# Performance work log

Hardware: AMD Instinct MI355X
Metric: run time of the kernel (lower is better)

Reference implementation:

```python
import jax, jax.numpy as jnp
import numpy as np

NEIGHBOR_RATE = 0.1  # neighbor_rate init arg
LEAKY_SLOPE = 0.2
NEG_INF = -1.0e9


def setup_inputs() -> dict:
    key = jax.random.key(0)
    k1, k2, k3, k4 = jax.random.split(key, 4)
    B, N, Din, H, hd = 4, 2048, 128, 4, 32  # output_dim = H*hd = 128
    h = jax.random.normal(k1, (B, N, Din), jnp.float32)
    adj = jax.random.uniform(k2, (B, N, N), jnp.float32)
    # stacked per-head params: W[k] in [Din, hd], a[k] in [2*hd]
    w_bound = 1.0 / np.sqrt(Din)
    a_bound = 1.0 / np.sqrt(2 * hd)
    W = jax.random.uniform(k3, (H, Din, hd), jnp.float32, -w_bound, w_bound)
    a = jax.random.uniform(k4, (H, 2 * hd), jnp.float32, -a_bound, a_bound)
    return {"h": h, "adj": adj, "W": W, "a": a}


def reference(h, adj, W, a):
    B, N, _ = h.shape
    H, _, hd = W.shape
    k = int(NEIGHBOR_RATE * N)  # num_neighbors
    # Wh: [B,H,N,hd]
    Wh = jnp.einsum('bnf,hfd->bhnd', h, W)
    # cat([Wh_i, Wh_j]) @ a  ==  Wh_i @ a[:hd] + Wh_j @ a[hd:] (broadcast trick)
    s_i = jnp.einsum('bhnd,hd->bhn', Wh, a[:, :hd])
    s_j = jnp.einsum('bhnd,hd->bhn', Wh, a[:, hd:])
    e = jax.nn.leaky_relu(s_i[..., :, None] + s_j[..., None, :], LEAKY_SLOPE)  # [B,H,N,N]
    # top-k mask along last (neighbor) axis, built by scatter like torch .scatter_
    _, idx = jax.lax.top_k(e, k)  # [B,H,N,k]
    row_mask = lambda i: jnp.zeros((N,), jnp.bool_).at[i].set(True)
    mask = jax.vmap(row_mask)(idx.reshape(-1, k)).reshape(e.shape)
    masked = jnp.where(mask, e, NEG_INF)
    attn = jax.nn.softmax(masked, axis=-1) * adj[:, None]  # [B,H,N,N]
    hp = jnp.einsum('bhnm,bhmd->bhnd', attn, Wh)
    # concat heads on feature dim -> [B,N,H*hd]
    return hp.transpose(0, 2, 1, 3).reshape(B, N, H * hd)
```

## Files before the change

### kernel.cpp

```cpp
#include <hip/hip_runtime.h>
#include <hip/hip_bf16.h>
#include <cmath>

#define BB 4
#define NN 2048
#define DIN 128
#define HH 4
#define HD 32
#define KSEL 204
#define BH (BB*HH)
#define KPAD 256
#define KST 264

typedef __attribute__((ext_vector_type(8))) short short8;
typedef __attribute__((ext_vector_type(4))) short short4v;
typedef __attribute__((ext_vector_type(4))) float float4v;

static __device__ inline short f2bf(float x) {
    __hip_bfloat16 b = __float2bfloat16(x);
    return __builtin_bit_cast(short, b);
}

typedef __attribute__((address_space(1))) const unsigned gq_t;
typedef __attribute__((address_space(3))) unsigned lq_t;
static __device__ inline void gload_lds16(const void* g, void* l) {
    __builtin_amdgcn_global_load_lds((gq_t*)g, (lq_t*)l, 16, 0, 0);
}

__global__ __launch_bounds__(256) void s_kernel(const float* __restrict__ h,
                                                const float* __restrict__ W,
                                                const float* __restrict__ a,
                                                float* __restrict__ si, float* __restrict__ sj) {
    __shared__ float w1L[HH][DIN], w2L[HH][DIN];
    int t = threadIdx.x;
    for (int e = t; e < 8 * DIN; e += 256) {
        int f = e & 127, v = e >> 7;
        int hh = v >> 1, half = v & 1;
        const float* Wp = W + ((size_t)hh * DIN + f) * HD;
        const float* ap = a + hh * 64 + half * 32;
        float acc = 0.f;
#pragma unroll
        for (int d = 0; d < 32; ++d) acc += Wp[d] * ap[d];
        if (half == 0) w1L[hh][f] = acc; else w2L[hh][f] = acc;
    }
    __syncthreads();

    int gid = blockIdx.x * 256 + t;
    int row = gid >> 2;
    int q   = gid & 3;
    int b = row >> 11, n = row & 2047;
    const float* hr = h + (size_t)row * DIN;

    float s1h0 = 0.f, s1h1 = 0.f, s1h2 = 0.f, s1h3 = 0.f;
    float s2h0 = 0.f, s2h1 = 0.f, s2h2 = 0.f, s2h3 = 0.f;
#pragma unroll
    for (int i = 0; i < 8; ++i) {
        int f = q * 4 + i * 16;
        float4 x = *(const float4*)(hr + f);
        const float* wa0 = &w1L[0][f]; const float* wb0 = &w2L[0][f];
        const float* wa1 = &w1L[1][f]; const float* wb1 = &w2L[1][f];
        const float* wa2 = &w1L[2][f]; const float* wb2 = &w2L[2][f];
        const float* wa3 = &w1L[3][f]; const float* wb3 = &w2L[3][f];
        s1h0 += x.x*wa0[0] + x.y*wa0[1] + x.z*wa0[2] + x.w*wa0[3];
        s2h0 += x.x*wb0[0] + x.y*wb0[1] + x.z*wb0[2] + x.w*wb0[3];
        s1h1 += x.x*wa1[0] + x.y*wa1[1] + x.z*wa1[2] + x.w*wa1[3];
        s2h1 += x.x*wb1[0] + x.y*wb1[1] + x.z*wb1[2] + x.w*wb1[3];
        s1h2 += x.x*wa2[0] + x.y*wa2[1] + x.z*wa2[2] + x.w*wa2[3];
        s2h2 += x.x*wb2[0] + x.y*wb2[1] + x.z*wb2[2] + x.w*wb2[3];
        s1h3 += x.x*wa3[0] + x.y*wa3[1] + x.z*wa3[2] + x.w*wa3[3];
        s2h3 += x.x*wb3[0] + x.y*wb3[1] + x.z*wb3[2] + x.w*wb3[3];
    }
#pragma unroll
    for (int off = 1; off <= 2; off <<= 1) {
        s1h0 += __shfl_xor(s1h0, off); s2h0 += __shfl_xor(s2h0, off);
        s1h1 += __shfl_xor(s1h1, off); s2h1 += __shfl_xor(s2h1, off);
        s1h2 += __shfl_xor(s1h2, off); s2h2 += __shfl_xor(s2h2, off);
        s1h3 += __shfl_xor(s1h3, off); s2h3 += __shfl_xor(s2h3, off);
    }
    float o1 = (q == 0) ? s1h0 : (q == 1) ? s1h1 : (q == 2) ? s1h2 : s1h3;
    float o2 = (q == 0) ? s2h0 : (q == 1) ? s2h1 : (q == 2) ? s2h2 : s2h3;
    size_t o = (size_t)(b * HH + q) * NN + n;
    si[o] = o1; sj[o] = o2;
}

__global__ __launch_bounds__(1024) void select_kernel(
        const float* __restrict__ h, const float* __restrict__ W,
        const float* __restrict__ sj,
        int* __restrict__ idxsel, float* __restrict__ sjsel,
        float* __restrict__ sjmax, short* __restrict__ Whsel) {
    int bh = blockIdx.x;
    int b = bh >> 2, hh = bh & 3;
    int t = threadIdx.x, lane = t & 63, w = t >> 6;
    __shared__ float sv[NN];
    __shared__ short WT[32][136];
    __shared__ int hist16[16][256];
    __shared__ int binInfo[2];
    __shared__ int wtot[4];
    __shared__ int wtotg[16], wtote[16], woffg[16], woffe[16];
    __shared__ float wmax[16];
    __shared__ int idxLDS[KSEL];

    for (int e = t; e < 32 * 128; e += 1024) {
        int n = e & 31, k = e >> 5;
        WT[n][k] = f2bf(W[(size_t)hh * (DIN * HD) + k * HD + n]);
    }

    const float* s = sj + (size_t)bh * NN;
    int j0 = t * 2;
    float2 xx = *(const float2*)(s + j0);
    sv[j0] = xx.x; sv[j0 + 1] = xx.y;
    unsigned u0 = __builtin_bit_cast(unsigned, xx.x);
    unsigned u1 = __builtin_bit_cast(unsigned, xx.y);
    u0 = (u0 & 0x80000000u) ? ~u0 : (u0 | 0x80000000u);
    u1 = (u1 & 0x80000000u) ? ~u1 : (u1 | 0x80000000u);
    float lmax = fmaxf(xx.x, xx.y);
#pragma unroll
    for (int off = 32; off >= 1; off >>= 1) lmax = fmaxf(lmax, __shfl_xor(lmax, off));
    if (lane == 0) wmax[w] = lmax;
    __syncthreads();
    if (t == 0) {
        float m = wmax[0];
#pragma unroll
        for (int i = 1; i < 16; ++i) m = fmaxf(m, wmax[i]);
        sjmax[bh] = m;
    }

    unsigned prefix = 0;
    int need = KSEL;
#pragma unroll
    for (int shift = 24; shift >= 0; shift -= 8) {
        ((int*)hist16)[t] = 0; ((int*)hist16)[t + 1024] = 0;
        ((int*)hist16)[t + 2048] = 0; ((int*)hist16)[t + 3072] = 0;
        __syncthreads();
        unsigned hmask = (shift < 24) ? (0xFFFFFFFFu << (shift + 8)) : 0u;
        if (((u0 ^ prefix) & hmask) == 0) atomicAdd(&hist16[w][(u0 >> shift) & 255], 1);
        if (((u1 ^ prefix) & hmask) == 0) atomicAdd(&hist16[w][(u1 >> shift) & 255], 1);
        __syncthreads();
        int sc = 0, hv = 0, bb = 0;
        if (t < 256) {
            bb = 255 - t;
            hv = 0;
#pragma unroll
            for (int i = 0; i < 16; ++i) hv += hist16[i][bb];
            sc = hv;
#pragma unroll
            for (int off = 1; off < 64; off <<= 1) {
                int u = __shfl_up(sc, off);
                if (lane >= off) sc += u;
            }
            if (lane == 63) wtot[w] = sc;
        }
        __syncthreads();
        if (t < 256) {
            int woffset = 0;
#pragma unroll
            for (int i = 0; i < 4; ++i) woffset += (i < w) ? wtot[i] : 0;
            int incl = sc + woffset;
            int excl = incl - hv;
            if (incl >= need && excl < need) {
                binInfo[0] = bb;
                binInfo[1] = excl;
            }
        }
        __syncthreads();
        prefix |= ((unsigned)binInfo[0]) << shift;
        need -= binInfo[1];
        __syncthreads();
    }
    unsigned T = prefix;
    int n_gt = KSEL - need;

    int cg = (u0 > T ? 1 : 0) + (u1 > T ? 1 : 0);
    int ce = (u0 == T ? 1 : 0) + (u1 == T ? 1 : 0);
    int sg = cg, se = ce;
#pragma unroll
    for (int off = 1; off < 64; off <<= 1) {
        int ug = __shfl_up(sg, off), ue = __shfl_up(se, off);
        if (lane >= off) { sg += ug; se += ue; }
    }
    if (lane == 63) { wtotg[w] = sg; wtote[w] = se; }
    __syncthreads();
    if (t == 0) {
        int rg = 0, re = 0;
#pragma unroll
        for (int i = 0; i < 16; ++i) {
            woffg[i] = rg; rg += wtotg[i];
            woffe[i] = re; re += wtote[i];
        }
    }
    __syncthreads();
    int pg = woffg[w] + sg - cg;
    int te = woffe[w] + se - ce;
    {
        unsigned kk[2] = {u0, u1};
#pragma unroll
        for (int r = 0; r < 2; ++r) {
            int j = j0 + r;
            if (kk[r] > T) {
                idxsel[bh * KSEL + pg] = j;
                sjsel[bh * KSEL + pg] = sv[j];
                idxLDS[pg] = j;
                pg++;
            } else if (kk[r] == T) {
                if (te < need) {
                    int pos = n_gt + te;
                    idxsel[bh * KSEL + pos] = j;
                    sjsel[bh * KSEL + pos] = sv[j];
                    idxLDS[pos] = j;
                }
                te++;
            }
        }
    }
    __syncthreads();

    {
        int mr = lane & 15, quad = lane >> 4;
        int jjp = w * 16 + mr;
        bool valid = jjp < KSEL;
        const float* hrow = h + ((size_t)b * NN + (valid ? idxLDS[jjp] : 0)) * DIN + quad * 8;
        float4v acc0 = {0.f, 0.f, 0.f, 0.f};
        float4v acc1 = {0.f, 0.f, 0.f, 0.f};
#pragma unroll
        for (int ks = 0; ks < 4; ++ks) {
            short8 afr;
            if (valid) {
                float4 xa = *(const float4*)(hrow + ks * 32);
                float4 xb = *(const float4*)(hrow + ks * 32 + 4);
                afr[0] = f2bf(xa.x); afr[1] = f2bf(xa.y); afr[2] = f2bf(xa.z); afr[3] = f2bf(xa.w);
                afr[4] = f2bf(xb.x); afr[5] = f2bf(xb.y); afr[6] = f2bf(xb.z); afr[7] = f2bf(xb.w);
            } else {
                afr = (short8){0, 0, 0, 0, 0, 0, 0, 0};
            }
            short8 b0 = *(const short8*)&WT[mr][ks * 32 + quad * 8];
            short8 b1 = *(const short8*)&WT[16 + mr][ks * 32 + quad * 8];
            acc0 = __builtin_amdgcn_mfma_f32_16x16x32_bf16(afr, b0, acc0, 0, 0, 0);
            acc1 = __builtin_amdgcn_mfma_f32_16x16x32_bf16(afr, b1, acc1, 0, 0, 0);
        }
        short4v o0, o1;
#pragma unroll
        for (int r = 0; r < 4; ++r) { o0[r] = f2bf(acc0[r]); o1[r] = f2bf(acc1[r]); }
        size_t base = (size_t)bh * HD * KPAD;
        int jjs = w * 16 + quad * 4;
        *(short4v*)&Whsel[base + (size_t)mr * KPAD + jjs] = o0;
        *(short4v*)&Whsel[base + (size_t)(16 + mr) * KPAD + jjs] = o1;
    }
}

__global__ __launch_bounds__(512) void attn2_kernel(
        const float* __restrict__ adj, const float* __restrict__ si,
        const int* __restrict__ idxsel, const float* __restrict__ sjsel,
        const float* __restrict__ sjmax, const short* __restrict__ Whsel,
        float* __restrict__ out) {
    int b = blockIdx.x >> 7;
    int tile = blockIdx.x & 127;
    __shared__ float adjbuf[2][2][NN];
    __shared__ short PSb[HH][16][KST];
    __shared__ int   idxS[HH][KPAD];
    __shared__ float sjS[HH][KPAD];
    __shared__ float invZS[HH][16];
    __shared__ float smaxS[HH];
    int t = threadIdx.x, w8 = t >> 6, lane = t & 63;
    int hh = w8 >> 1, g = w8 & 1;
    int mr = lane & 15, quad = lane >> 4;

    int i0 = tile * 16;
    const char* adjb = (const char*)(adj + (size_t)b * NN * NN + (size_t)i0 * NN);

    for (int e = t; e < HH * KPAD; e += 512) {
        int h2 = e >> 8, jj = e & 255;
        bool v = jj < KSEL;
        idxS[h2][jj] = v ? idxsel[(b * HH + h2) * KSEL + jj] : 0;
        sjS[h2][jj]  = v ? sjsel[(b * HH + h2) * KSEL + jj] : -1e30f;
    }
    if (t < HH) smaxS[t] = sjmax[b * HH + t];

    short8 bfr[8];
    {
        const short* wp = Whsel + (size_t)((b * HH + hh) * HD) * KPAD;
#pragma unroll
        for (int ks = 0; ks < 8; ++ks)
            bfr[ks] = *(const short8*)(wp + (size_t)(g * 16 + mr) * KPAD + ks * 32 + quad * 8);
    }
    int bh = b * HH + hh;
    float sivAll = (lane < 8) ? si[(size_t)bh * NN + i0 + 2 * lane + g] : 0.f;

    __syncthreads();

    {
        int lx = lane << 4, off = w8 << 10;
        gload_lds16(adjb + off + lx,              (char*)&adjbuf[0][0][0] + off);
        gload_lds16(adjb + 8192 + off + lx,       (char*)&adjbuf[0][0][0] + 8192 + off);
        gload_lds16(adjb + 16384 + off + lx,      (char*)&adjbuf[1][0][0] + off);
        gload_lds16(adjb + 24576 + off + lx,      (char*)&adjbuf[1][0][0] + 8192 + off);
    }
    asm volatile("s_waitcnt vmcnt(2)" ::: "memory");
    __builtin_amdgcn_sched_barrier(0);
    __builtin_amdgcn_s_barrier();

    float smax = smaxS[hh];
    for (int s = 0; s < 8; ++s) {
        int cur = s & 1;
        if (s >= 1 && s < 7) {
            const char* gs = adjb + (size_t)(s + 1) * 16384;
            char* lb = (char*)&adjbuf[cur ^ 1][0][0];
            int lx = lane << 4, off = w8 << 10;
            gload_lds16(gs + off + lx,        lb + off);
            gload_lds16(gs + 8192 + off + lx, lb + 8192 + off);
        }
        {
            int i_loc = 2 * s + g;
            float siv = __shfl(sivAll, s);
            float m = siv + smax;
            m = (m >= 0.f) ? m : 0.2f * m;
            float z = 0.f;
            short* prow = &PSb[hh][i_loc][0];
#pragma unroll
            for (int k = 0; k < 2; ++k) {
                int jj = k * 128 + lane * 2;
                int ja = idxS[hh][jj], jb = idxS[hh][jj + 1];
                float ava = adjbuf[cur][g][ja], avb = adjbuf[cur][g][jb];
                float ea = siv + sjS[hh][jj];
                float eb = siv + sjS[hh][jj + 1];
                ea = (ea >= 0.f) ? ea : 0.2f * ea;
                eb = (eb >= 0.f) ? eb : 0.2f * eb;
                float ca = __expf(ea - m);
                float cb = __expf(eb - m);
                z += ca + cb;
                short2 p;
                p.x = f2bf(ca * ava);
                p.y = f2bf(cb * avb);
                *(short2*)&prow[jj] = p;
            }
#pragma unroll
            for (int off = 32; off >= 1; off >>= 1) z += __shfl_xor(z, off);
            if (lane == 0) invZS[hh][i_loc] = 1.0f / z;
        }
        if (s < 7) {
            asm volatile("s_waitcnt vmcnt(0)" ::: "memory");
            __builtin_amdgcn_sched_barrier(0);
            __builtin_amdgcn_s_barrier();
        }
    }
    __syncthreads();

    {
        float4v acc = {0.f, 0.f, 0.f, 0.f};
#pragma unroll
        for (int ks = 0; ks < 8; ++ks) {
            short8 afr = *(const short8*)&PSb[hh][mr][ks * 32 + quad * 8];
            acc = __builtin_amdgcn_mfma_f32_16x16x32_bf16(afr, bfr[ks], acc, 0, 0, 0);
        }
#pragma unroll
        for (int r = 0; r < 4; ++r) {
            int i_loc = quad * 4 + r;
            int d = g * 16 + mr;
            out[((size_t)(b * NN + i0 + i_loc)) * (HH * HD) + hh * HD + d] =
                acc[r] * invZS[hh][i_loc];
        }
    }
}

extern "C" void kernel_launch(void* const* d_in, const int* in_sizes, int n_in,
                              void* d_out, int out_size, void* d_ws, size_t ws_size,
                              hipStream_t stream) {
    const float* h   = (const float*)d_in[0];
    const float* adj = (const float*)d_in[1];
    const float* W   = (const float*)d_in[2];
    const float* a   = (const float*)d_in[3];
    float* out = (float*)d_out;

    float* si     = (float*)d_ws;
    float* sj     = si + (size_t)BH * NN;
    float* sjsel  = sj + (size_t)BH * NN;
    float* sjmax  = sjsel + (size_t)BH * KSEL;
    int*   idxsel = (int*)(sjmax + 16);
    short* Whsel  = (short*)(idxsel + (size_t)BH * KSEL);

    s_kernel<<<128, 256, 0, stream>>>(h, W, a, si, sj);
    select_kernel<<<BH, 1024, 0, stream>>>(h, W, sj, idxsel, sjsel, sjmax, Whsel);
    attn2_kernel<<<BB * 128, 512, 0, stream>>>(adj, si, idxsel, sjsel, sjmax, Whsel, out);
}
```

Measured before the change: 126.5 us.

## Deepen adj prefetch to 4-slot ring, split rows across wave pair

Replaces the double-buffered two-row adj staging with a four-slot ring of single rows, keeping three loads in flight and waiting with graded vmcnt counts. Each row is now processed by both waves of a head, each handling half the selected neighbors, and the partial softmax denominators are combined at output time. The intent is to hide global-load latency better and spread the gather work more evenly. In exchange it runs twice as many barrier-separated steps and fully unrolls the loop.

```diff
diff --git a/kernel.cpp b/kernel.cpp
--- a/kernel.cpp
+++ b/kernel.cpp
@@ -254,11 +254,11 @@
         float* __restrict__ out) {
     int b = blockIdx.x >> 7;
     int tile = blockIdx.x & 127;
-    __shared__ float adjbuf[2][2][NN];
+    __shared__ float adjbuf[4][NN];
     __shared__ short PSb[HH][16][KST];
     __shared__ int   idxS[HH][KPAD];
     __shared__ float sjS[HH][KPAD];
-    __shared__ float invZS[HH][16];
+    __shared__ float zpartS[HH][16][2];
     __shared__ float smaxS[HH];
     int t = threadIdx.x, w8 = t >> 6, lane = t & 63;
     int hh = w8 >> 1, g = w8 & 1;
@@ -283,61 +283,55 @@
             bfr[ks] = *(const short8*)(wp + (size_t)(g * 16 + mr) * KPAD + ks * 32 + quad * 8);
     }
     int bh = b * HH + hh;
-    float sivAll = (lane < 8) ? si[(size_t)bh * NN + i0 + 2 * lane + g] : 0.f;
+    float sivAll = (lane < 16) ? si[(size_t)bh * NN + i0 + lane] : 0.f;
 
     __syncthreads();
 
     {
         int lx = lane << 4, off = w8 << 10;
-        gload_lds16(adjb + off + lx,              (char*)&adjbuf[0][0][0] + off);
-        gload_lds16(adjb + 8192 + off + lx,       (char*)&adjbuf[0][0][0] + 8192 + off);
-        gload_lds16(adjb + 16384 + off + lx,      (char*)&adjbuf[1][0][0] + off);
-        gload_lds16(adjb + 24576 + off + lx,      (char*)&adjbuf[1][0][0] + 8192 + off);
+        gload_lds16(adjb + off + lx,         (char*)&adjbuf[0][0] + off);
+        gload_lds16(adjb + 8192 + off + lx,  (char*)&adjbuf[1][0] + off);
+        gload_lds16(adjb + 16384 + off + lx, (char*)&adjbuf[2][0] + off);
     }
     asm volatile("s_waitcnt vmcnt(2)" ::: "memory");
     __builtin_amdgcn_sched_barrier(0);
     __builtin_amdgcn_s_barrier();
 
     float smax = smaxS[hh];
-    for (int s = 0; s < 8; ++s) {
-        int cur = s & 1;
-        if (s >= 1 && s < 7) {
-            const char* gs = adjb + (size_t)(s + 1) * 16384;
-            char* lb = (char*)&adjbuf[cur ^ 1][0][0];
+#pragma unroll
+    for (int s = 0; s < 16; ++s) {
+        int cur = s & 3;
+        if (s < 13) {
             int lx = lane << 4, off = w8 << 10;
-            gload_lds16(gs + off + lx,        lb + off);
-            gload_lds16(gs + 8192 + off + lx, lb + 8192 + off);
+            gload_lds16(adjb + (size_t)(s + 3) * 8192 + off + lx,
+                        (char*)&adjbuf[(s + 3) & 3][0] + off);
         }
         {
-            int i_loc = 2 * s + g;
             float siv = __shfl(sivAll, s);
             float m = siv + smax;
             m = (m >= 0.f) ? m : 0.2f * m;
-            float z = 0.f;
-            short* prow = &PSb[hh][i_loc][0];
-#pragma unroll
-            for (int k = 0; k < 2; ++k) {
-                int jj = k * 128 + lane * 2;
-                int ja = idxS[hh][jj], jb = idxS[hh][jj + 1];
-                float ava = adjbuf[cur][g][ja], avb = adjbuf[cur][g][jb];
-                float ea = siv + sjS[hh][jj];
-                float eb = siv + sjS[hh][jj + 1];
-                ea = (ea >= 0.f) ? ea : 0.2f * ea;
-                eb = (eb >= 0.f) ? eb : 0.2f * eb;
-                float ca = __expf(ea - m);
-                float cb = __expf(eb - m);
-                z += ca + cb;
-                short2 p;
-                p.x = f2bf(ca * ava);
-                p.y = f2bf(cb * avb);
-                *(short2*)&prow[jj] = p;
-            }
+            int jj = g * 128 + lane * 2;
+            int ja = idxS[hh][jj], jb = idxS[hh][jj + 1];
+            float ava = adjbuf[cur][ja], avb = adjbuf[cur][jb];
+            float ea = siv + sjS[hh][jj];
+            float eb = siv + sjS[hh][jj + 1];
+            ea = (ea >= 0.f) ? ea : 0.2f * ea;
+            eb = (eb >= 0.f) ? eb : 0.2f * eb;
+            float ca = __expf(ea - m);
+            float cb = __expf(eb - m);
+            float z = ca + cb;
+            short2 p;
+            p.x = f2bf(ca * ava);
+            p.y = f2bf(cb * avb);
+            *(short2*)&PSb[hh][s][jj] = p;
 #pragma unroll
             for (int off = 32; off >= 1; off >>= 1) z += __shfl_xor(z, off);
-            if (lane == 0) invZS[hh][i_loc] = 1.0f / z;
-        }
-        if (s < 7) {
-            asm volatile("s_waitcnt vmcnt(0)" ::: "memory");
+            if (lane == 0) zpartS[hh][s][g] = z;
+        }
+        if (s < 15) {
+            if (s <= 12)      { asm volatile("s_waitcnt vmcnt(2)" ::: "memory"); }
+            else if (s == 13) { asm volatile("s_waitcnt vmcnt(1)" ::: "memory"); }
+            else              { asm volatile("s_waitcnt vmcnt(0)" ::: "memory"); }
             __builtin_amdgcn_sched_barrier(0);
             __builtin_amdgcn_s_barrier();
         }
@@ -354,9 +348,10 @@
 #pragma unroll
         for (int r = 0; r < 4; ++r) {
             int i_loc = quad * 4 + r;
+            float invZ = 1.0f / (zpartS[hh][i_loc][0] + zpartS[hh][i_loc][1]);
             int d = g * 16 + mr;
             out[((size_t)(b * NN + i0 + i_loc)) * (HH * HD) + hh * HD + d] =
-                acc[r] * invZS[hh][i_loc];
+                acc[r] * invZ;
         }
     }
 }
```

After: 132.4 us. 4.7% more time.
